# Optimization experiments

Hardware: AMD Instinct MI355X
Metric: run time of the kernel (lower is better)

Reference implementation:

```python
import jax, jax.numpy as jnp
import numpy as np

EPS = 1e-5
MASK_VALUE = -1000000000.0


def _pw(x, w):
    # 1x1 conv: [B,C,T,F] x [O,C] -> [B,O,T,F]
    return jnp.einsum('bctf,oc->botf', x, w)


def _bn_prelu(y, g, b, m, v, a):
    # eval-mode BatchNorm2d followed by PReLU (single shared slope)
    scale = (g / jnp.sqrt(v + EPS))[None, :, None, None]
    y = (y - m[None, :, None, None]) * scale + b[None, :, None, None]
    return jnp.where(y >= 0, y, a[0] * y)


def setup_inputs() -> dict:
    key = jax.random.key(0)
    ks = jax.random.split(key, 12)
    B, C, T, F = 2, 128, 512, 256
    C4 = C // 4
    d = {}
    d['x'] = jax.random.normal(ks[0], (B, C, T, F), jnp.float32)
    d['w1'] = jax.random.normal(ks[1], (C4, C), jnp.float32) * (1.0 / np.sqrt(C))
    d['g1'] = jnp.ones((C4,), jnp.float32)
    d['b1'] = jnp.zeros((C4,), jnp.float32)
    d['m1'] = jax.random.normal(ks[2], (C4,), jnp.float32) * 0.1
    d['v1'] = jax.random.uniform(ks[3], (C4,), jnp.float32, 0.5, 1.5)
    d['a1'] = jnp.full((1,), 0.25, jnp.float32)
    d['w2'] = jax.random.normal(ks[4], (C4, C), jnp.float32) * (1.0 / np.sqrt(C))
    d['g2'] = jnp.ones((C4,), jnp.float32)
    d['b2'] = jnp.zeros((C4,), jnp.float32)
    d['m2'] = jax.random.normal(ks[5], (C4,), jnp.float32) * 0.1
    d['v2'] = jax.random.uniform(ks[6], (C4,), jnp.float32, 0.5, 1.5)
    d['a2'] = jnp.full((1,), 0.25, jnp.float32)
    d['w3'] = jax.random.normal(ks[7], (C, C4), jnp.float32) * (1.0 / np.sqrt(C4))
    d['g3'] = jnp.ones((C,), jnp.float32)
    d['b3'] = jnp.zeros((C,), jnp.float32)
    d['m3'] = jax.random.normal(ks[8], (C,), jnp.float32) * 0.1
    d['v3'] = jax.random.uniform(ks[9], (C,), jnp.float32, 0.5, 1.5)
    d['a3'] = jnp.full((1,), 0.25, jnp.float32)
    return d


def reference(x, w1, g1, b1, m1, v1, a1, w2, g2, b2, m2, v2, a2,
              w3, g3, b3, m3, v3, a3):
    B, C, T, F = x.shape
    # --- frequency-axis attention (non-causal) ---
    x1 = _bn_prelu(_pw(x, w1), g1, b1, m1, v1, a1)          # [B,C/4,T,F]
    sf = jnp.einsum('bctf,bctg->btfg', x1, x1) / np.float32(np.sqrt(C * F / 2))
    af = jax.nn.softmax(sf, axis=-1)                         # [B,T,F,F]
    of = jnp.einsum('btfg,bctg->btfc', af, x1)               # [B,T,F,C/4]
    # --- time-axis attention (causal) ---
    x2 = _bn_prelu(_pw(x, w2), g2, b2, m2, v2, a2)           # [B,C/4,T,F]
    st = jnp.einsum('bctf,bcsf->bfts', x2, x2) / np.float32(np.sqrt(C * T / 2))
    i = jnp.arange(T)
    mask = jnp.where(i[:, None] >= i[None, :], 0.0, MASK_VALUE).astype(st.dtype)
    at = jax.nn.softmax(st + mask[None, None, :, :], axis=-1)  # [B,F,T,T]
    # combine: causal time attention applied to frequency-attended values
    m = jnp.einsum('bfts,bsfc->bftc', at, of)                # [B,F,T,C/4]
    m = m.transpose(0, 3, 2, 1)                              # [B,C/4,T,F]
    m = _bn_prelu(_pw(m, w3), g3, b3, m3, v3, a3)            # [B,C,T,F]
    return m + x
```

## Files before the change

### kernel.cpp

```cpp
#include <hip/hip_runtime.h>
#include <hip/hip_bf16.h>

typedef __hip_bfloat16 bf16;
typedef __bf16 bfv8 __attribute__((ext_vector_type(8)));
typedef float f32x4 __attribute__((ext_vector_type(4)));

#define HD __device__ __forceinline__

constexpr int Bb = 2, Cc = 128, C4 = 32, Tt = 512, Ff = 256;
constexpr float EPSf = 1e-5f;
constexpr float SCALE1 = 1.0f / 128.0f;
constexpr float SCALE2 = 0.005524271728019903f;
constexpr float NEG_BIG = -1.0e30f;
constexpr size_t SLAB = (size_t)Bb * Tt * C4 * Ff;

HD float b2f(bf16 h) { return __bfloat162float(h); }
HD bf16 f2b(float f) { return __float2bfloat16(f); }
HD float lo16(unsigned u) { return __uint_as_float(u << 16); }
HD float hi16(unsigned u) { return __uint_as_float(u & 0xffff0000u); }
HD unsigned short f2b_bits(float f) {
    union { bf16 h; unsigned short s; } u; u.h = __float2bfloat16(f); return u.s;
}
HD unsigned pack2f(float a, float b) {
    return (unsigned)f2b_bits(a) | ((unsigned)f2b_bits(b) << 16);
}

HD f32x4 mfma_bf16(uint4 a, uint4 b, f32x4 c) {
    return __builtin_amdgcn_mfma_f32_16x16x32_bf16(
        __builtin_bit_cast(bfv8, a), __builtin_bit_cast(bfv8, b), c, 0, 0, 0);
}

__global__ void kFlag(const unsigned* __restrict__ g1w, int* __restrict__ flag)
{
    if (threadIdx.x == 0 && blockIdx.x == 0)
        *flag = (g1w[0] == 0x3F800000u) ? 1 : 0;
}

__global__ __launch_bounds__(256) void kA(
    const void* __restrict__ x,
    const void* __restrict__ w1, const void* __restrict__ g1, const void* __restrict__ be1,
    const void* __restrict__ mu1, const void* __restrict__ va1, const void* __restrict__ a1,
    const void* __restrict__ w2, const void* __restrict__ g2, const void* __restrict__ be2,
    const void* __restrict__ mu2, const void* __restrict__ va2, const void* __restrict__ a2,
    const int* __restrict__ flag,
    bf16* __restrict__ x1w, bf16* __restrict__ x2w)
{
    __shared__ float bnsc[64], bnsh[64];
    __shared__ float alsh[2];
    int tid = threadIdx.x;
    int f32 = *flag;

    if (tid < 64) {
        int o = tid; float g, be, mm, vv;
        if (f32) {
            if (o < 32) {
                g = ((const float*)g1)[o]; be = ((const float*)be1)[o];
                mm = ((const float*)mu1)[o]; vv = ((const float*)va1)[o];
            } else {
                int q = o - 32;
                g = ((const float*)g2)[q]; be = ((const float*)be2)[q];
                mm = ((const float*)mu2)[q]; vv = ((const float*)va2)[q];
            }
        } else {
            if (o < 32) {
                g = b2f(((const bf16*)g1)[o]); be = b2f(((const bf16*)be1)[o]);
                mm = b2f(((const bf16*)mu1)[o]); vv = b2f(((const bf16*)va1)[o]);
            } else {
                int q = o - 32;
                g = b2f(((const bf16*)g2)[q]); be = b2f(((const bf16*)be2)[q]);
                mm = b2f(((const bf16*)mu2)[q]); vv = b2f(((const bf16*)va2)[q]);
            }
        }
        float sc = g / sqrtf(vv + EPSf);
        bnsc[tid] = sc; bnsh[tid] = be - mm * sc;
    }
    if (tid == 0) {
        if (f32) { alsh[0] = ((const float*)a1)[0]; alsh[1] = ((const float*)a2)[0]; }
        else     { alsh[0] = b2f(((const bf16*)a1)[0]); alsh[1] = b2f(((const bf16*)a2)[0]); }
    }
    __syncthreads();

    int b = blockIdx.x / Tt;
    int t = blockIdx.x % Tt;
    int wv = tid >> 6, l = tid & 63;
    int lc = l & 15, lg = l >> 4;
    int fb = wv * 64;
    const size_t TF = (size_t)Tt * Ff;

    f32x4 acc[4][4];
#pragma unroll
    for (int ft = 0; ft < 4; ++ft)
#pragma unroll
        for (int ot = 0; ot < 4; ++ot) acc[ft][ot] = (f32x4){0.f, 0.f, 0.f, 0.f};

    size_t xrow = (size_t)b * Cc * TF + (size_t)t * Ff;

    for (int kc = 0; kc < 4; ++kc) {
        int c0 = kc * 32 + 8 * lg;
        uint4 whi[4], wlo[4];
        if (f32) {
#pragma unroll
            for (int ot = 0; ot < 4; ++ot) {
                int o = ot * 16 + lc;
                const float* wr = ((o < 32) ? (const float*)w1 + (size_t)o * 128
                                            : (const float*)w2 + (size_t)(o - 32) * 128) + c0;
                float4 v0 = *(const float4*)wr;
                float4 v1 = *(const float4*)(wr + 4);
                float v[8] = {v0.x, v0.y, v0.z, v0.w, v1.x, v1.y, v1.z, v1.w};
                unsigned hw[4], lw[4];
#pragma unroll
                for (int j = 0; j < 4; ++j) {
                    unsigned short h0 = f2b_bits(v[2 * j]), h1 = f2b_bits(v[2 * j + 1]);
                    float r0 = v[2 * j] - lo16((unsigned)h0);
                    float r1 = v[2 * j + 1] - lo16((unsigned)h1);
                    hw[j] = (unsigned)h0 | ((unsigned)h1 << 16);
                    lw[j] = (unsigned)f2b_bits(r0) | ((unsigned)f2b_bits(r1) << 16);
                }
                whi[ot] = *(const uint4*)hw;
                wlo[ot] = *(const uint4*)lw;
            }
        } else {
#pragma unroll
            for (int ot = 0; ot < 4; ++ot) {
                int o = ot * 16 + lc;
                const bf16* wr = ((o < 32) ? (const bf16*)w1 + (size_t)o * 128
                                           : (const bf16*)w2 + (size_t)(o - 32) * 128) + c0;
                whi[ot] = *(const uint4*)wr;
            }
        }
#pragma unroll
        for (int ft = 0; ft < 4; ++ft) {
            int f = fb + ft * 16 + lc;
            size_t xoff = xrow + (size_t)c0 * TF + f;
            if (f32) {
                const float* xp = (const float*)x + xoff;
                float v[8];
#pragma unroll
                for (int j = 0; j < 8; ++j) v[j] = xp[(size_t)j * TF];
                unsigned hb[4], lb[4];
#pragma unroll
                for (int j = 0; j < 4; ++j) {
                    unsigned short h0 = f2b_bits(v[2 * j]), h1 = f2b_bits(v[2 * j + 1]);
                    float r0 = v[2 * j] - lo16((unsigned)h0);
                    float r1 = v[2 * j + 1] - lo16((unsigned)h1);
                    hb[j] = (unsigned)h0 | ((unsigned)h1 << 16);
                    lb[j] = (unsigned)f2b_bits(r0) | ((unsigned)f2b_bits(r1) << 16);
                }
                uint4 bhx = *(const uint4*)hb;
                uint4 blx = *(const uint4*)lb;
#pragma unroll
                for (int ot = 0; ot < 4; ++ot) {
                    acc[ft][ot] = mfma_bf16(whi[ot], bhx, acc[ft][ot]);
                    acc[ft][ot] = mfma_bf16(whi[ot], blx, acc[ft][ot]);
                    acc[ft][ot] = mfma_bf16(wlo[ot], bhx, acc[ft][ot]);
                }
            } else {
                const unsigned short* xp = (const unsigned short*)x + xoff;
                unsigned u[4];
#pragma unroll
                for (int j = 0; j < 4; ++j)
                    u[j] = (unsigned)xp[(size_t)(2 * j) * TF]
                         | ((unsigned)xp[(size_t)(2 * j + 1) * TF] << 16);
                uint4 bx = *(const uint4*)u;
#pragma unroll
                for (int ot = 0; ot < 4; ++ot)
                    acc[ft][ot] = mfma_bf16(whi[ot], bx, acc[ft][ot]);
            }
        }
    }

    float al1 = alsh[0], al2 = alsh[1];
#pragma unroll
    for (int ft = 0; ft < 4; ++ft) {
        int f = fb + ft * 16 + lc;
#pragma unroll
        for (int ot = 0; ot < 4; ++ot) {
            f32x4 a = acc[ft][ot];
            int ob = ot * 16 + 4 * lg;
            float y[4];
#pragma unroll
            for (int r = 0; r < 4; ++r) {
                int o = ob + r;
                float al = (o < 32) ? al1 : al2;
                float yy = a[r] * bnsc[o] + bnsh[o];
                y[r] = (yy >= 0.f) ? yy : al * yy;
            }
            uint2 pv = make_uint2(pack2f(y[0], y[1]), pack2f(y[2], y[3]));
            if (ot < 2) {
                bf16* p = x1w + ((size_t)(b * Tt + t) * Ff + f) * 32 + ob;
                *(uint2*)p = pv;
            } else {
                bf16* p = x2w + ((size_t)(b * Ff + f) * Tt + t) * 32 + (ob - 32);
                *(uint2*)p = pv;
            }
        }
    }
}

__global__ __launch_bounds__(256) void kB(const bf16* __restrict__ x1w,
                                          bf16* __restrict__ ofw)
{
    __shared__ __align__(16) unsigned short Vt[32 * 264];
    __shared__ __align__(16) unsigned short Pb[4 * 16 * 40];
    int tid = threadIdx.x;
    int b = blockIdx.x >> 9;
    int t = blockIdx.x & 511;
    const bf16* hb = x1w + ((size_t)(b * Tt + t) * Ff) * 32;

    {
        const uint4* src = (const uint4*)(hb + (size_t)tid * 32);
        uint4 q0 = src[0], q1 = src[1], q2 = src[2], q3 = src[3];
        unsigned vals[16] = { q0.x, q0.y, q0.z, q0.w, q1.x, q1.y, q1.z, q1.w,
                              q2.x, q2.y, q2.z, q2.w, q3.x, q3.y, q3.z, q3.w };
#pragma unroll
        for (int cc = 0; cc < 16; ++cc) {
            Vt[(2 * cc) * 264 + tid]     = (unsigned short)(vals[cc] & 0xffffu);
            Vt[(2 * cc + 1) * 264 + tid] = (unsigned short)(vals[cc] >> 16);
        }
    }
    __syncthreads();

    int w = tid >> 6, l = tid & 63;
    int lc = l & 15, lg = l >> 4;
    unsigned short* Pw = &Pb[w * 640];

    for (int ch = w; ch < 16; ch += 4) {
        int f0 = ch * 16;
        uint4 qa = *(const uint4*)(hb + (size_t)(f0 + lc) * 32 + 8 * lg);
        f32x4 accA = {0.f, 0.f, 0.f, 0.f};
        f32x4 accB = {0.f, 0.f, 0.f, 0.f};
        float mx[4] = {NEG_BIG, NEG_BIG, NEG_BIG, NEG_BIG};
        float ls[4] = {0.f, 0.f, 0.f, 0.f};

        for (int g0 = 0; g0 < 256; g0 += 32) {
            uint4 kb0 = *(const uint4*)(hb + (size_t)(g0 + lc) * 32 + 8 * lg);
            uint4 kb1 = *(const uint4*)(hb + (size_t)(g0 + 16 + lc) * 32 + 8 * lg);
            f32x4 z = {0.f, 0.f, 0.f, 0.f};
            f32x4 sA = mfma_bf16(qa, kb0, z);
            f32x4 sB = mfma_bf16(qa, kb1, z);

            float cm[4];
#pragma unroll
            for (int r = 0; r < 4; ++r) {
                sA[r] *= SCALE1; sB[r] *= SCALE1;
                cm[r] = fmaxf(sA[r], sB[r]);
            }
#pragma unroll
            for (int msk = 1; msk < 16; msk <<= 1)
#pragma unroll
                for (int r = 0; r < 4; ++r)
                    cm[r] = fmaxf(cm[r], __shfl_xor(cm[r], msk));

            float p0[4], p1[4], rs[4];
#pragma unroll
            for (int r = 0; r < 4; ++r) {
                float nm = fmaxf(mx[r], cm[r]);
                float al = __expf(mx[r] - nm);
                p0[r] = __expf(sA[r] - nm);
                p1[r] = __expf(sB[r] - nm);
                mx[r] = nm;
                rs[r] = p0[r] + p1[r];
                ls[r] *= al;
                accA[r] *= al; accB[r] *= al;
            }
#pragma unroll
            for (int msk = 1; msk < 16; msk <<= 1)
#pragma unroll
                for (int r = 0; r < 4; ++r)
                    rs[r] += __shfl_xor(rs[r], msk);
#pragma unroll
            for (int r = 0; r < 4; ++r) ls[r] += rs[r];

#pragma unroll
            for (int r = 0; r < 4; ++r) {
                Pw[(4 * lg + r) * 40 + lc]      = f2b_bits(p0[r]);
                Pw[(4 * lg + r) * 40 + 16 + lc] = f2b_bits(p1[r]);
            }
            uint4 pa  = *(const uint4*)&Pw[lc * 40 + 8 * lg];
            uint4 vb0 = *(const uint4*)&Vt[lc * 264 + g0 + 8 * lg];
            uint4 vb1 = *(const uint4*)&Vt[(16 + lc) * 264 + g0 + 8 * lg];
            accA = mfma_bf16(pa, vb0, accA);
            accB = mfma_bf16(pa, vb1, accB);
        }

        bf16* ob = ofw + ((size_t)(b * Tt + t) * Ff + f0) * 32;
#pragma unroll
        for (int r = 0; r < 4; ++r) {
            float inv = 1.f / ls[r];
            int fr = 4 * lg + r;
            ob[(size_t)fr * 32 + lc]      = f2b(accA[r] * inv);
            ob[(size_t)fr * 32 + 16 + lc] = f2b(accB[r] * inv);
        }
    }
}

__global__ __launch_bounds__(512) void kC(const bf16* __restrict__ x2w,
                                          const bf16* __restrict__ ofw,
                                          bf16* __restrict__ mtw)
{
    __shared__ __align__(16) unsigned short Vt[32 * 520];
    __shared__ __align__(16) unsigned short Pb[8 * 16 * 40];
    int tid = threadIdx.x;
    int b = blockIdx.x >> 8;
    int f = blockIdx.x & 255;
    const bf16* kb = x2w + ((size_t)(b * Ff + f) * Tt) * 32;

    {
        const uint4* src = (const uint4*)(ofw + ((size_t)(b * Tt + tid) * Ff + f) * 32);
        uint4 q0 = src[0], q1 = src[1], q2 = src[2], q3 = src[3];
        unsigned vals[16] = { q0.x, q0.y, q0.z, q0.w, q1.x, q1.y, q1.z, q1.w,
                              q2.x, q2.y, q2.z, q2.w, q3.x, q3.y, q3.z, q3.w };
#pragma unroll
        for (int cc = 0; cc < 16; ++cc) {
            Vt[(2 * cc) * 520 + tid]     = (unsigned short)(vals[cc] & 0xffffu);
            Vt[(2 * cc + 1) * 520 + tid] = (unsigned short)(vals[cc] >> 16);
        }
    }
    __syncthreads();

    int w = tid >> 6, l = tid & 63;
    int lc = l & 15, lg = l >> 4;
    unsigned short* Pw = &Pb[w * 640];

    for (int ch = w; ch < 32; ch += 8) {
        int t0 = ch * 16;
        uint4 qa = *(const uint4*)(kb + (size_t)(t0 + lc) * 32 + 8 * lg);
        f32x4 accA = {0.f, 0.f, 0.f, 0.f};
        f32x4 accB = {0.f, 0.f, 0.f, 0.f};
        float mx[4] = {NEG_BIG, NEG_BIG, NEG_BIG, NEG_BIG};
        float ls[4] = {0.f, 0.f, 0.f, 0.f};

        for (int s0 = 0; s0 < t0 + 16; s0 += 32) {
            uint4 kb0 = *(const uint4*)(kb + (size_t)(s0 + lc) * 32 + 8 * lg);
            uint4 kb1 = *(const uint4*)(kb + (size_t)(s0 + 16 + lc) * 32 + 8 * lg);
            f32x4 z = {0.f, 0.f, 0.f, 0.f};
            f32x4 sA = mfma_bf16(qa, kb0, z);
            f32x4 sB = mfma_bf16(qa, kb1, z);

            float cm[4];
#pragma unroll
            for (int r = 0; r < 4; ++r) {
                int tg = t0 + 4 * lg + r;
                sA[r] = (s0 + lc <= tg)      ? sA[r] * SCALE2 : NEG_BIG;
                sB[r] = (s0 + 16 + lc <= tg) ? sB[r] * SCALE2 : NEG_BIG;
                cm[r] = fmaxf(sA[r], sB[r]);
            }
#pragma unroll
            for (int msk = 1; msk < 16; msk <<= 1)
#pragma unroll
                for (int r = 0; r < 4; ++r)
                    cm[r] = fmaxf(cm[r], __shfl_xor(cm[r], msk));

            float p0[4], p1[4], rs[4];
#pragma unroll
            for (int r = 0; r < 4; ++r) {
                float nm = fmaxf(mx[r], cm[r]);
                float al = __expf(mx[r] - nm);
                p0[r] = __expf(sA[r] - nm);
                p1[r] = __expf(sB[r] - nm);
                mx[r] = nm;
                rs[r] = p0[r] + p1[r];
                ls[r] *= al;
                accA[r] *= al; accB[r] *= al;
            }
#pragma unroll
            for (int msk = 1; msk < 16; msk <<= 1)
#pragma unroll
                for (int r = 0; r < 4; ++r)
                    rs[r] += __shfl_xor(rs[r], msk);
#pragma unroll
            for (int r = 0; r < 4; ++r) ls[r] += rs[r];

#pragma unroll
            for (int r = 0; r < 4; ++r) {
                Pw[(4 * lg + r) * 40 + lc]      = f2b_bits(p0[r]);
                Pw[(4 * lg + r) * 40 + 16 + lc] = f2b_bits(p1[r]);
            }
            uint4 pa  = *(const uint4*)&Pw[lc * 40 + 8 * lg];
            uint4 vb0 = *(const uint4*)&Vt[lc * 520 + s0 + 8 * lg];
            uint4 vb1 = *(const uint4*)&Vt[(16 + lc) * 520 + s0 + 8 * lg];
            accA = mfma_bf16(pa, vb0, accA);
            accB = mfma_bf16(pa, vb1, accB);
        }

#pragma unroll
        for (int r = 0; r < 4; ++r) {
            float inv = 1.f / ls[r];
            int tr = t0 + 4 * lg + r;
            bf16* ob = mtw + ((size_t)(b * Tt + tr) * Ff + f) * 32;
            ob[lc]      = f2b(accA[r] * inv);
            ob[16 + lc] = f2b(accB[r] * inv);
        }
    }
}

__global__ __launch_bounds__(256) void kD(
    const bf16* __restrict__ mtw, const void* __restrict__ xg,
    const void* __restrict__ w3, const void* __restrict__ g3, const void* __restrict__ be3,
    const void* __restrict__ mu3, const void* __restrict__ va3, const void* __restrict__ a3,
    const int* __restrict__ flag,
    void* __restrict__ out)
{
    __shared__ __align__(16) uint4 Whi[8 * 64];
    __shared__ __align__(16) uint4 Wlo[8 * 64];
    __shared__ float sc3[128], sh3[128];
    __shared__ float alsh;
    int tid = threadIdx.x;
    int f32 = *flag;

    for (int e = tid; e < 512; e += 256) {
        int cht = e >> 6, le = e & 63;
        int elc = le & 15, elg = le >> 4;
        int ch = cht * 16 + elc;
        if (f32) {
            const float* wr = (const float*)w3 + ch * 32 + 8 * elg;
            unsigned hw[4], lw[4];
#pragma unroll
            for (int j = 0; j < 4; ++j) {
                float a = wr[2 * j], c2 = wr[2 * j + 1];
                unsigned short ah = f2b_bits(a), ch2 = f2b_bits(c2);
                float ar = a - lo16((unsigned)ah);
                float cr = c2 - lo16((unsigned)ch2);
                hw[j] = (unsigned)ah | ((unsigned)ch2 << 16);
                lw[j] = (unsigned)f2b_bits(ar) | ((unsigned)f2b_bits(cr) << 16);
            }
            Whi[e] = *(const uint4*)hw;
            Wlo[e] = *(const uint4*)lw;
        } else {
            const bf16* wr = (const bf16*)w3 + ch * 32 + 8 * elg;
            Whi[e] = *(const uint4*)wr;
            Wlo[e] = make_uint4(0u, 0u, 0u, 0u);
        }
    }
    if (f32) {
        if (tid < 128) {
            float g = ((const float*)g3)[tid], be = ((const float*)be3)[tid];
            float mm = ((const float*)mu3)[tid], vv = ((const float*)va3)[tid];
            float s = g / sqrtf(vv + EPSf);
            sc3[tid] = s; sh3[tid] = be - mm * s;
        }
        if (tid == 0) alsh = ((const float*)a3)[0];
    } else {
        if (tid < 128) {
            float g = b2f(((const bf16*)g3)[tid]), be = b2f(((const bf16*)be3)[tid]);
            float mm = b2f(((const bf16*)mu3)[tid]), vv = b2f(((const bf16*)va3)[tid]);
            float s = g / sqrtf(vv + EPSf);
            sc3[tid] = s; sh3[tid] = be - mm * s;
        }
        if (tid == 0) alsh = b2f(((const bf16*)a3)[0]);
    }
    __syncthreads();

    int wv = tid >> 6, l = tid & 63;
    int lc = l & 15, lg = l >> 4;

    uint4 bhi[8], blo[8];
#pragma unroll
    for (int c = 0; c < 8; ++c) { bhi[c] = Whi[c * 64 + l]; blo[c] = Wlo[c * 64 + l]; }

    int b = blockIdx.x >> 10;
    int posb = (blockIdx.x & 1023) * 128;
    float al3 = alsh;

    const float* xgf = (const float*)xg;
    const bf16* xgb = (const bf16*)xg;
    float* outf = (float*)out;
    bf16* outb = (bf16*)out;

    for (int pi = 0; pi < 2; ++pi) {
        int prow = posb + (2 * wv + pi) * 16;
        uint4 afrag = ((const uint4*)(mtw + ((size_t)b * 131072 + prow + lc) * 32))[lg];
        size_t gbase = (size_t)b * ((size_t)128 * 131072) + (size_t)(prow + 4 * lg);

        if (f32) {
            float4 xv[8];
#pragma unroll
            for (int c = 0; c < 8; ++c) {
                size_t gi = (gbase + (size_t)(c * 16 + lc) * 131072) >> 2;
                xv[c] = ((const float4*)xgf)[gi];
            }
#pragma unroll
            for (int c = 0; c < 8; ++c) {
                f32x4 z = {0.f, 0.f, 0.f, 0.f};
                f32x4 acc = mfma_bf16(afrag, blo[c], z);
                acc = mfma_bf16(afrag, bhi[c], acc);
                int ch = c * 16 + lc;
                float sc = sc3[ch], sh = sh3[ch];
                float4 r;
                float y0 = acc[0] * sc + sh; y0 = (y0 >= 0.f) ? y0 : al3 * y0;
                float y1 = acc[1] * sc + sh; y1 = (y1 >= 0.f) ? y1 : al3 * y1;
                float y2 = acc[2] * sc + sh; y2 = (y2 >= 0.f) ? y2 : al3 * y2;
                float y3 = acc[3] * sc + sh; y3 = (y3 >= 0.f) ? y3 : al3 * y3;
                r.x = y0 + xv[c].x; r.y = y1 + xv[c].y;
                r.z = y2 + xv[c].z; r.w = y3 + xv[c].w;
                size_t gi = (gbase + (size_t)ch * 131072) >> 2;
                ((float4*)outf)[gi] = r;
            }
        } else {
            uint2 xv[8];
#pragma unroll
            for (int c = 0; c < 8; ++c) {
                size_t gi = (gbase + (size_t)(c * 16 + lc) * 131072) >> 2;
                xv[c] = ((const uint2*)xgb)[gi];
            }
#pragma unroll
            for (int c = 0; c < 8; ++c) {
                f32x4 z = {0.f, 0.f, 0.f, 0.f};
                f32x4 acc = mfma_bf16(afrag, blo[c], z);
                acc = mfma_bf16(afrag, bhi[c], acc);
                int ch = c * 16 + lc;
                float sc = sc3[ch], sh = sh3[ch];
                float y0 = acc[0] * sc + sh; y0 = (y0 >= 0.f) ? y0 : al3 * y0;
                float y1 = acc[1] * sc + sh; y1 = (y1 >= 0.f) ? y1 : al3 * y1;
                float y2 = acc[2] * sc + sh; y2 = (y2 >= 0.f) ? y2 : al3 * y2;
                float y3 = acc[3] * sc + sh; y3 = (y3 >= 0.f) ? y3 : al3 * y3;
                uint2 r;
                r.x = pack2f(y0 + lo16(xv[c].x), y1 + hi16(xv[c].x));
                r.y = pack2f(y2 + lo16(xv[c].y), y3 + hi16(xv[c].y));
                size_t gi = (gbase + (size_t)ch * 131072) >> 2;
                ((uint2*)outb)[gi] = r;
            }
        }
    }
}

extern "C" void kernel_launch(void* const* d_in, const int* in_sizes, int n_in,
                              void* d_out, int out_size, void* d_ws, size_t ws_size,
                              hipStream_t stream)
{
    (void)in_sizes; (void)n_in; (void)out_size; (void)ws_size;
    const void* x  = d_in[0];
    const void* w1 = d_in[1];
    const void* g1 = d_in[2];
    const void* b1 = d_in[3];
    const void* m1 = d_in[4];
    const void* v1 = d_in[5];
    const void* a1 = d_in[6];
    const void* w2 = d_in[7];
    const void* g2 = d_in[8];
    const void* b2 = d_in[9];
    const void* m2 = d_in[10];
    const void* v2 = d_in[11];
    const void* a2 = d_in[12];
    const void* w3 = d_in[13];
    const void* g3 = d_in[14];
    const void* b3 = d_in[15];
    const void* m3 = d_in[16];
    const void* v3 = d_in[17];
    const void* a3 = d_in[18];

    bf16* base = (bf16*)d_ws;
    bf16* x1w = base;
    bf16* x2w = base + SLAB;
    bf16* ofw = base + 2 * SLAB;
    bf16* mtw = base;
    int* flag = (int*)(base + 3 * SLAB);

    kFlag<<<1, 64, 0, stream>>>((const unsigned*)g1, flag);
    kA<<<Bb * Tt, 256, 0, stream>>>(x, w1, g1, b1, m1, v1, a1,
                                    w2, g2, b2, m2, v2, a2, flag, x1w, x2w);
    kB<<<Bb * Tt, 256, 0, stream>>>(x1w, ofw);
    kC<<<Bb * Ff, 512, 0, stream>>>(x2w, ofw, mtw);
    kD<<<(Bb * Tt * Ff) / 128, 256, 0, stream>>>(mtw, x, w3, g3, b3, m3, v3, a3, flag, d_out);
}
```

Before: 496.6 us.

## Transpose attention MFMAs and use single-pass softmax in frequency attention

Swaps MFMA operand order so each lane owns one query row, which makes softmax row reductions need only two cross-lane shuffles instead of four-step butterflies per element. The frequency-attention kernel now computes all 256 scores up front and does an exact one-pass softmax with no online rescaling. The time-attention kernel processes 64-key blocks, applies the causal mask only on boundary blocks, and uses exp2 with a prescaled log2e constant. P is staged through a padded 64-bit LDS layout and outputs are written as packed vector stores. These changes raise register pressure and add branch divergence in the causal loop.

```diff
diff --git a/kernel.cpp b/kernel.cpp
--- a/kernel.cpp
+++ b/kernel.cpp
@@ -4,6 +4,7 @@
 typedef __hip_bfloat16 bf16;
 typedef __bf16 bfv8 __attribute__((ext_vector_type(8)));
 typedef float f32x4 __attribute__((ext_vector_type(4)));
+typedef unsigned long long u64;
 
 #define HD __device__ __forceinline__
 
@@ -11,6 +12,7 @@
 constexpr float EPSf = 1e-5f;
 constexpr float SCALE1 = 1.0f / 128.0f;
 constexpr float SCALE2 = 0.005524271728019903f;
+constexpr float LOG2E  = 1.44269504088896340736f;
 constexpr float NEG_BIG = -1.0e30f;
 constexpr size_t SLAB = (size_t)Bb * Tt * C4 * Ff;
 
@@ -23,6 +25,9 @@
 }
 HD unsigned pack2f(float a, float b) {
     return (unsigned)f2b_bits(a) | ((unsigned)f2b_bits(b) << 16);
+}
+HD u64 pack4f(float a, float b, float c, float d) {
+    return (u64)pack2f(a, b) | ((u64)pack2f(c, d) << 32);
 }
 
 HD f32x4 mfma_bf16(uint4 a, uint4 b, f32x4 c) {
@@ -201,7 +206,7 @@
                                           bf16* __restrict__ ofw)
 {
     __shared__ __align__(16) unsigned short Vt[32 * 264];
-    __shared__ __align__(16) unsigned short Pb[4 * 16 * 40];
+    __shared__ __align__(16) u64 P2[4 * 64 * 17];
     int tid = threadIdx.x;
     int b = blockIdx.x >> 9;
     int t = blockIdx.x & 511;
@@ -222,75 +227,79 @@
 
     int w = tid >> 6, l = tid & 63;
     int lc = l & 15, lg = l >> 4;
-    unsigned short* Pw = &Pb[w * 640];
+    u64* Pw = &P2[w * 64 * 17];
+    const float K1 = SCALE1 * LOG2E;
 
     for (int ch = w; ch < 16; ch += 4) {
         int f0 = ch * 16;
         uint4 qa = *(const uint4*)(hb + (size_t)(f0 + lc) * 32 + 8 * lg);
-        f32x4 accA = {0.f, 0.f, 0.f, 0.f};
-        f32x4 accB = {0.f, 0.f, 0.f, 0.f};
-        float mx[4] = {NEG_BIG, NEG_BIG, NEG_BIG, NEG_BIG};
-        float ls[4] = {0.f, 0.f, 0.f, 0.f};
-
-        for (int g0 = 0; g0 < 256; g0 += 32) {
+
+        f32x4 sA[8], sB[8];
+#pragma unroll
+        for (int m = 0; m < 8; ++m) {
+            int g0 = 32 * m;
             uint4 kb0 = *(const uint4*)(hb + (size_t)(g0 + lc) * 32 + 8 * lg);
             uint4 kb1 = *(const uint4*)(hb + (size_t)(g0 + 16 + lc) * 32 + 8 * lg);
             f32x4 z = {0.f, 0.f, 0.f, 0.f};
-            f32x4 sA = mfma_bf16(qa, kb0, z);
-            f32x4 sB = mfma_bf16(qa, kb1, z);
-
-            float cm[4];
+            sA[m] = mfma_bf16(kb0, qa, z);
+            sB[m] = mfma_bf16(kb1, qa, z);
+        }
+
+        f32x4 vm = sA[0];
+#pragma unroll
+        for (int m = 0; m < 8; ++m) {
 #pragma unroll
             for (int r = 0; r < 4; ++r) {
-                sA[r] *= SCALE1; sB[r] *= SCALE1;
-                cm[r] = fmaxf(sA[r], sB[r]);
-            }
-#pragma unroll
-            for (int msk = 1; msk < 16; msk <<= 1)
-#pragma unroll
-                for (int r = 0; r < 4; ++r)
-                    cm[r] = fmaxf(cm[r], __shfl_xor(cm[r], msk));
-
-            float p0[4], p1[4], rs[4];
-#pragma unroll
-            for (int r = 0; r < 4; ++r) {
-                float nm = fmaxf(mx[r], cm[r]);
-                float al = __expf(mx[r] - nm);
-                p0[r] = __expf(sA[r] - nm);
-                p1[r] = __expf(sB[r] - nm);
-                mx[r] = nm;
-                rs[r] = p0[r] + p1[r];
-                ls[r] *= al;
-                accA[r] *= al; accB[r] *= al;
-            }
-#pragma unroll
-            for (int msk = 1; msk < 16; msk <<= 1)
-#pragma unroll
-                for (int r = 0; r < 4; ++r)
-                    rs[r] += __shfl_xor(rs[r], msk);
-#pragma unroll
-            for (int r = 0; r < 4; ++r) ls[r] += rs[r];
-
-#pragma unroll
-            for (int r = 0; r < 4; ++r) {
-                Pw[(4 * lg + r) * 40 + lc]      = f2b_bits(p0[r]);
-                Pw[(4 * lg + r) * 40 + 16 + lc] = f2b_bits(p1[r]);
-            }
-            uint4 pa  = *(const uint4*)&Pw[lc * 40 + 8 * lg];
-            uint4 vb0 = *(const uint4*)&Vt[lc * 264 + g0 + 8 * lg];
-            uint4 vb1 = *(const uint4*)&Vt[(16 + lc) * 264 + g0 + 8 * lg];
-            accA = mfma_bf16(pa, vb0, accA);
-            accB = mfma_bf16(pa, vb1, accB);
-        }
-
-        bf16* ob = ofw + ((size_t)(b * Tt + t) * Ff + f0) * 32;
-#pragma unroll
-        for (int r = 0; r < 4; ++r) {
-            float inv = 1.f / ls[r];
-            int fr = 4 * lg + r;
-            ob[(size_t)fr * 32 + lc]      = f2b(accA[r] * inv);
-            ob[(size_t)fr * 32 + 16 + lc] = f2b(accB[r] * inv);
-        }
+                if (m > 0) vm[r] = fmaxf(vm[r], sA[m][r]);
+                vm[r] = fmaxf(vm[r], sB[m][r]);
+            }
+        }
+        float mx = fmaxf(fmaxf(vm[0], vm[1]), fmaxf(vm[2], vm[3]));
+        mx = fmaxf(mx, __shfl_xor(mx, 16));
+        mx = fmaxf(mx, __shfl_xor(mx, 32));
+        float mk = mx * K1;
+
+        float sum = 0.f;
+#pragma unroll
+        for (int m = 0; m < 8; ++m) {
+            float a0 = exp2f(fmaf(sA[m][0], K1, -mk));
+            float a1 = exp2f(fmaf(sA[m][1], K1, -mk));
+            float a2 = exp2f(fmaf(sA[m][2], K1, -mk));
+            float a3 = exp2f(fmaf(sA[m][3], K1, -mk));
+            float b0 = exp2f(fmaf(sB[m][0], K1, -mk));
+            float b1 = exp2f(fmaf(sB[m][1], K1, -mk));
+            float b2 = exp2f(fmaf(sB[m][2], K1, -mk));
+            float b3 = exp2f(fmaf(sB[m][3], K1, -mk));
+            sum += (a0 + a1) + (a2 + a3) + (b0 + b1) + (b2 + b3);
+            Pw[(8 * m + lg) * 17 + lc]     = pack4f(a0, a1, a2, a3);
+            Pw[(8 * m + 4 + lg) * 17 + lc] = pack4f(b0, b1, b2, b3);
+        }
+        sum += __shfl_xor(sum, 16);
+        sum += __shfl_xor(sum, 32);
+
+        f32x4 accA = {0.f, 0.f, 0.f, 0.f};
+        f32x4 accB = {0.f, 0.f, 0.f, 0.f};
+#pragma unroll
+        for (int m = 0; m < 8; ++m) {
+            int g0 = 32 * m;
+            uint4 va0 = *(const uint4*)&Vt[lc * 264 + g0 + 8 * lg];
+            uint4 va1 = *(const uint4*)&Vt[(16 + lc) * 264 + g0 + 8 * lg];
+            u64 lo = Pw[(8 * m + 2 * lg) * 17 + lc];
+            u64 hi = Pw[(8 * m + 2 * lg + 1) * 17 + lc];
+            uint4 pb = make_uint4((unsigned)lo, (unsigned)(lo >> 32),
+                                  (unsigned)hi, (unsigned)(hi >> 32));
+            accA = mfma_bf16(va0, pb, accA);
+            accB = mfma_bf16(va1, pb, accB);
+        }
+
+        float invl = 1.f / sum;
+        bf16* ob = ofw + ((size_t)(b * Tt + t) * Ff + f0 + lc) * 32;
+        uint2 wA = make_uint2(pack2f(accA[0] * invl, accA[1] * invl),
+                              pack2f(accA[2] * invl, accA[3] * invl));
+        uint2 wB = make_uint2(pack2f(accB[0] * invl, accB[1] * invl),
+                              pack2f(accB[2] * invl, accB[3] * invl));
+        *(uint2*)(ob + 4 * lg) = wA;
+        *(uint2*)(ob + 16 + 4 * lg) = wB;
     }
 }
 
@@ -299,7 +308,7 @@
                                           bf16* __restrict__ mtw)
 {
     __shared__ __align__(16) unsigned short Vt[32 * 520];
-    __shared__ __align__(16) unsigned short Pb[8 * 16 * 40];
+    __shared__ __align__(16) u64 P2[8 * 16 * 17];
     int tid = threadIdx.x;
     int b = blockIdx.x >> 8;
     int f = blockIdx.x & 255;
@@ -320,77 +329,106 @@
 
     int w = tid >> 6, l = tid & 63;
     int lc = l & 15, lg = l >> 4;
-    unsigned short* Pw = &Pb[w * 640];
+    u64* Pw = &P2[w * 16 * 17];
+    const float K2 = SCALE2 * LOG2E;
 
     for (int ch = w; ch < 32; ch += 8) {
         int t0 = ch * 16;
+        int send = t0 + 16;
         uint4 qa = *(const uint4*)(kb + (size_t)(t0 + lc) * 32 + 8 * lg);
         f32x4 accA = {0.f, 0.f, 0.f, 0.f};
         f32x4 accB = {0.f, 0.f, 0.f, 0.f};
-        float mx[4] = {NEG_BIG, NEG_BIG, NEG_BIG, NEG_BIG};
-        float ls[4] = {0.f, 0.f, 0.f, 0.f};
-
-        for (int s0 = 0; s0 < t0 + 16; s0 += 32) {
-            uint4 kb0 = *(const uint4*)(kb + (size_t)(s0 + lc) * 32 + 8 * lg);
-            uint4 kb1 = *(const uint4*)(kb + (size_t)(s0 + 16 + lc) * 32 + 8 * lg);
-            f32x4 z = {0.f, 0.f, 0.f, 0.f};
-            f32x4 sA = mfma_bf16(qa, kb0, z);
-            f32x4 sB = mfma_bf16(qa, kb1, z);
-
-            float cm[4];
-#pragma unroll
-            for (int r = 0; r < 4; ++r) {
-                int tg = t0 + 4 * lg + r;
-                sA[r] = (s0 + lc <= tg)      ? sA[r] * SCALE2 : NEG_BIG;
-                sB[r] = (s0 + 16 + lc <= tg) ? sB[r] * SCALE2 : NEG_BIG;
-                cm[r] = fmaxf(sA[r], sB[r]);
-            }
-#pragma unroll
-            for (int msk = 1; msk < 16; msk <<= 1)
+        float mr = NEG_BIG, ls = 0.f;
+        int tt = t0 + lc;
+
+        for (int s0 = 0; s0 < send; s0 += 64) {
+            int nmv = ((send - s0) > 32) ? 2 : 1;
+            int bnd = (s0 + 64 > t0);
+            f32x4 sA[2], sB[2];
+
+#pragma unroll
+            for (int m = 0; m < 2; ++m) {
+                if (m < nmv) {
+                    int g0 = s0 + 32 * m;
+                    uint4 kb0 = *(const uint4*)(kb + (size_t)(g0 + lc) * 32 + 8 * lg);
+                    uint4 kb1 = *(const uint4*)(kb + (size_t)(g0 + 16 + lc) * 32 + 8 * lg);
+                    f32x4 z = {0.f, 0.f, 0.f, 0.f};
+                    sA[m] = mfma_bf16(kb0, qa, z);
+                    sB[m] = mfma_bf16(kb1, qa, z);
+                    if (bnd) {
+#pragma unroll
+                        for (int r = 0; r < 4; ++r) {
+                            sA[m][r] = (g0 + 4 * lg + r <= tt)      ? sA[m][r] : NEG_BIG;
+                            sB[m][r] = (g0 + 16 + 4 * lg + r <= tt) ? sB[m][r] : NEG_BIG;
+                        }
+                    }
+                }
+            }
+
+            f32x4 vm = sA[0];
+#pragma unroll
+            for (int r = 0; r < 4; ++r) vm[r] = fmaxf(vm[r], sB[0][r]);
+            if (nmv == 2) {
 #pragma unroll
                 for (int r = 0; r < 4; ++r)
-                    cm[r] = fmaxf(cm[r], __shfl_xor(cm[r], msk));
-
-            float p0[4], p1[4], rs[4];
-#pragma unroll
-            for (int r = 0; r < 4; ++r) {
-                float nm = fmaxf(mx[r], cm[r]);
-                float al = __expf(mx[r] - nm);
-                p0[r] = __expf(sA[r] - nm);
-                p1[r] = __expf(sB[r] - nm);
-                mx[r] = nm;
-                rs[r] = p0[r] + p1[r];
-                ls[r] *= al;
-                accA[r] *= al; accB[r] *= al;
-            }
-#pragma unroll
-            for (int msk = 1; msk < 16; msk <<= 1)
-#pragma unroll
-                for (int r = 0; r < 4; ++r)
-                    rs[r] += __shfl_xor(rs[r], msk);
-#pragma unroll
-            for (int r = 0; r < 4; ++r) ls[r] += rs[r];
-
-#pragma unroll
-            for (int r = 0; r < 4; ++r) {
-                Pw[(4 * lg + r) * 40 + lc]      = f2b_bits(p0[r]);
-                Pw[(4 * lg + r) * 40 + 16 + lc] = f2b_bits(p1[r]);
-            }
-            uint4 pa  = *(const uint4*)&Pw[lc * 40 + 8 * lg];
-            uint4 vb0 = *(const uint4*)&Vt[lc * 520 + s0 + 8 * lg];
-            uint4 vb1 = *(const uint4*)&Vt[(16 + lc) * 520 + s0 + 8 * lg];
-            accA = mfma_bf16(pa, vb0, accA);
-            accB = mfma_bf16(pa, vb1, accB);
-        }
-
-#pragma unroll
-        for (int r = 0; r < 4; ++r) {
-            float inv = 1.f / ls[r];
-            int tr = t0 + 4 * lg + r;
-            bf16* ob = mtw + ((size_t)(b * Tt + tr) * Ff + f) * 32;
-            ob[lc]      = f2b(accA[r] * inv);
-            ob[16 + lc] = f2b(accB[r] * inv);
-        }
+                    vm[r] = fmaxf(vm[r], fmaxf(sA[1][r], sB[1][r]));
+            }
+            float gm = fmaxf(fmaxf(vm[0], vm[1]), fmaxf(vm[2], vm[3]));
+            gm = fmaxf(gm, __shfl_xor(gm, 16));
+            gm = fmaxf(gm, __shfl_xor(gm, 32));
+
+            float nm = fmaxf(mr, gm);
+            float al = exp2f((mr - nm) * K2);
+            mr = nm;
+            float mk = nm * K2;
+#pragma unroll
+            for (int r = 0; r < 4; ++r) { accA[r] *= al; accB[r] *= al; }
+
+            float ts = 0.f;
+#pragma unroll
+            for (int m = 0; m < 2; ++m) {
+                if (m < nmv) {
+                    float a0 = exp2f(fmaf(sA[m][0], K2, -mk));
+                    float a1 = exp2f(fmaf(sA[m][1], K2, -mk));
+                    float a2 = exp2f(fmaf(sA[m][2], K2, -mk));
+                    float a3 = exp2f(fmaf(sA[m][3], K2, -mk));
+                    float b0 = exp2f(fmaf(sB[m][0], K2, -mk));
+                    float b1 = exp2f(fmaf(sB[m][1], K2, -mk));
+                    float b2 = exp2f(fmaf(sB[m][2], K2, -mk));
+                    float b3 = exp2f(fmaf(sB[m][3], K2, -mk));
+                    ts += (a0 + a1) + (a2 + a3) + (b0 + b1) + (b2 + b3);
+                    Pw[(8 * m + lg) * 17 + lc]     = pack4f(a0, a1, a2, a3);
+                    Pw[(8 * m + 4 + lg) * 17 + lc] = pack4f(b0, b1, b2, b3);
+                }
+            }
+            ts += __shfl_xor(ts, 16);
+            ts += __shfl_xor(ts, 32);
+            ls = ls * al + ts;
+
+#pragma unroll
+            for (int m = 0; m < 2; ++m) {
+                if (m < nmv) {
+                    int g0 = s0 + 32 * m;
+                    uint4 va0 = *(const uint4*)&Vt[lc * 520 + g0 + 8 * lg];
+                    uint4 va1 = *(const uint4*)&Vt[(16 + lc) * 520 + g0 + 8 * lg];
+                    u64 lo = Pw[(8 * m + 2 * lg) * 17 + lc];
+                    u64 hi = Pw[(8 * m + 2 * lg + 1) * 17 + lc];
+                    uint4 pb = make_uint4((unsigned)lo, (unsigned)(lo >> 32),
+                                          (unsigned)hi, (unsigned)(hi >> 32));
+                    accA = mfma_bf16(va0, pb, accA);
+                    accB = mfma_bf16(va1, pb, accB);
+                }
+            }
+        }
+
+        float invl = 1.f / ls;
+        bf16* ob = mtw + (((size_t)(b * Tt + t0 + lc) * Ff + f)) * 32;
+        uint2 wA = make_uint2(pack2f(accA[0] * invl, accA[1] * invl),
+                              pack2f(accA[2] * invl, accA[3] * invl));
+        uint2 wB = make_uint2(pack2f(accB[0] * invl, accB[1] * invl),
+                              pack2f(accB[2] * invl, accB[3] * invl));
+        *(uint2*)(ob + 4 * lg) = wA;
+        *(uint2*)(ob + 16 + 4 * lg) = wB;
     }
 }
 
```

New measurement: 439.5 us. 11.5% less time.
